# Kernel tuning notes

Hardware: AMD Instinct MI355X
Metric: run time of the kernel (lower is better)

The kernel has to match this reference:

```python
import jax, jax.numpy as jnp
import numpy as np

N_FREQ = 48  # tcnn Frequency encoding n_frequencies


def _freq_encode(x):
    # x: [N,3] in [0,1]; tcnn Frequency: sin/cos of x * 2^f * pi, f=0..F-1
    freqs = (2.0 ** jnp.arange(N_FREQ, dtype=jnp.float32)) * jnp.pi  # [F]
    ang = x[:, :, None] * freqs  # [N,3,F]
    enc = jnp.stack([jnp.sin(ang), jnp.cos(ang)], axis=-1)  # [N,3,F,2]
    return enc.reshape(x.shape[0], -1)  # [N, 3*F*2]


def _bilinear_sample(plane, coords):
    # plane: [R,R,F] (H,W,feat); coords: [N,2] in [-1,1], coords[:,0]->width(x), coords[:,1]->height(y)
    # matches torch grid_sample(align_corners=True, bilinear) for in-range coords
    R = plane.shape[0]
    gx = (coords[:, 0] + 1.0) * 0.5 * (R - 1)
    gy = (coords[:, 1] + 1.0) * 0.5 * (R - 1)
    x0f = jnp.clip(jnp.floor(gx), 0.0, R - 1)
    y0f = jnp.clip(jnp.floor(gy), 0.0, R - 1)
    x0 = x0f.astype(jnp.int32)
    y0 = y0f.astype(jnp.int32)
    x1 = jnp.minimum(x0 + 1, R - 1)
    y1 = jnp.minimum(y0 + 1, R - 1)
    wx = (gx - x0f)[:, None]
    wy = (gy - y0f)[:, None]
    v00 = plane[y0, x0]
    v01 = plane[y0, x1]
    v10 = plane[y1, x0]
    v11 = plane[y1, x1]
    return (v00 * (1 - wx) * (1 - wy) + v01 * wx * (1 - wy)
            + v10 * (1 - wx) * wy + v11 * wx * wy)  # [N,F]


def setup_inputs() -> dict:
    key = jax.random.key(0)
    ks = jax.random.split(key, 8)
    N = 524288
    res, fdim = 32, 16
    enc_dim = 3 * N_FREQ * 2  # 288
    d_in = enc_dim + fdim     # 304
    h = 64
    positions = jax.random.uniform(ks[0], (N, 3), dtype=jnp.float32)
    aabb = jnp.array([0.0, 0.0, 0.0, 1.0, 1.0, 1.0], dtype=jnp.float32)
    triplane = jax.random.normal(ks[1], (3, res, res, fdim), dtype=jnp.float32) * 0.001
    W0 = jax.random.normal(ks[2], (d_in, h), dtype=jnp.float32) / np.sqrt(d_in)
    W1 = jax.random.normal(ks[3], (h, h), dtype=jnp.float32) / np.sqrt(h)
    W2 = jax.random.normal(ks[4], (h, h), dtype=jnp.float32) / np.sqrt(h)
    W3 = jax.random.normal(ks[5], (h, 4), dtype=jnp.float32) / np.sqrt(h)
    return {"positions": positions, "aabb": aabb, "triplane": triplane,
            "W0": W0, "W1": W1, "W2": W2, "W3": W3}


def reference(positions, aabb, triplane, W0, W1, W2, W3):
    aabb_min, aabb_max = aabb[:3], aabb[3:]
    xn = (positions - aabb_min) / (aabb_max - aabb_min)          # normalized [0,1]
    sc = 2.0 * xn - 1.0                                          # scaled_coords in [-1,1]
    selector = jnp.all((xn > 0.0) & (xn < 1.0), axis=-1)
    # plane coordinate pairs as in the torch code
    coords = jnp.stack([
        jnp.stack([sc[:, 0], sc[:, 1]], axis=1),  # xy
        jnp.stack([sc[:, 0], sc[:, 2]], axis=1),  # xz
        jnp.stack([sc[:, 1], sc[:, 2]], axis=1),  # zy
    ], axis=0)  # [3,N,2]
    feats = jax.vmap(_bilinear_sample)(triplane, coords).sum(0)  # [N,fdim]
    h = jnp.concatenate([_freq_encode(xn), feats], axis=1)       # [N,304]
    h = jnp.sin(h @ W0)
    h = jnp.sin(h @ W1)
    h = jnp.sin(h @ W2)
    out = h @ W3                                                 # [N,4]
    rgb = jax.nn.sigmoid(out[:, :3])
    density = jnp.exp(out[:, 3:4] - 1.0) * selector[:, None]     # trunc_exp(x-1)
    return rgb, density
```

## Files before the change

kernel.cpp:

```cpp
#include <hip/hip_runtime.h>
#include <stdint.h>

typedef _Float16 half8  __attribute__((ext_vector_type(8)));
typedef _Float16 half2v __attribute__((ext_vector_type(2)));
typedef float f32x4 __attribute__((ext_vector_type(4)));

#define TPW 8
#define WPB 8
#define NT  512

__device__ __forceinline__ half2v pkrtz(float a, float b) {
    return __builtin_bit_cast(half2v, __builtin_amdgcn_cvt_pkrtz(a, b));
}

static __device__ __forceinline__ void wave_fence() {
    __builtin_amdgcn_wave_barrier();
    asm volatile("" ::: "memory");
}

__device__ __forceinline__ float bf2f(uint16_t u) {
    return __uint_as_float(((uint32_t)u) << 16);
}
__device__ __forceinline__ uint16_t f2bf(float f) {
    uint32_t u = __float_as_uint(f);
    u = (u + 0x7FFFu + ((u >> 16) & 1u)) >> 16;
    return (uint16_t)u;
}

template<bool BF>
__device__ __forceinline__ float lde(const void* p, uint32_t i) {
    if constexpr (BF) return bf2f(((const uint16_t*)p)[i]);
    else              return ((const float*)p)[i];
}
template<bool BF>
__device__ __forceinline__ void st1(void* p, uint32_t i, float v) {
    if constexpr (BF) ((uint16_t*)p)[i] = f2bf(v);
    else              ((float*)p)[i] = v;
}
template<bool BF>
__device__ __forceinline__ void ld8(const void* p, uint32_t i, float* o) {
    if constexpr (BF) {
        const uint4 c = *(const uint4*)((const uint16_t*)p + i);
        const uint32_t* pu = (const uint32_t*)&c;
#pragma unroll
        for (int j = 0; j < 4; ++j) {
            o[2 * j]     = __uint_as_float(pu[j] << 16);
            o[2 * j + 1] = __uint_as_float(pu[j] & 0xFFFF0000u);
        }
    } else {
        const float4 a = *(const float4*)((const float*)p + i);
        const float4 b = *(const float4*)((const float*)p + i + 4);
        o[0] = a.x; o[1] = a.y; o[2] = a.z; o[3] = a.w;
        o[4] = b.x; o[5] = b.y; o[6] = b.z; o[7] = b.w;
    }
}

__device__ __forceinline__ int hswz(int p, int g) {
    return p * 72 + ((g + 2 * (p >> 2)) & 7) * 8;
}

template<bool BF>
__device__ __forceinline__ void run_all(
    const void* __restrict__ posg, const void* __restrict__ aabbg,
    const void* __restrict__ tpg,
    const void* __restrict__ w0g, const void* __restrict__ w1g,
    const void* __restrict__ w2g, const void* __restrict__ w3g,
    void* __restrict__ outp, int npts,
    _Float16* w0t, _Float16* w1t, _Float16* w2t, _Float16* w3t, _Float16* hbuf)
{
    const int tid = threadIdx.x;
    const float I2PI = 0.15915494309189535f;

    for (int e = tid; e < 64 * 24; e += NT) { int n = e / 24, k = 304 + e % 24; w0t[n * 328 + k] = (_Float16)0.0f; }
    for (int e = tid; e < 4 * 72; e += NT) w3t[e] = (_Float16)0.0f;
    for (int e = tid; e < 304 * 64; e += NT) { int k = e >> 6, n = e & 63; w0t[n * 328 + k] = (_Float16)(lde<BF>(w0g, e) * I2PI); }
    for (int e = tid; e < 64 * 64;  e += NT) { int k = e >> 6, n = e & 63; w1t[n * 72 + k] = (_Float16)(lde<BF>(w1g, e) * I2PI);
                                               w2t[n * 72 + k] = (_Float16)(lde<BF>(w2g, e) * I2PI); }
    __syncthreads();
    for (int e = tid; e < 64 * 4;   e += NT) { int k = e >> 2, n = e & 3;  w3t[n * 72 + k] = (_Float16)lde<BF>(w3g, e); }
    __syncthreads();

    const int w = tid >> 6, lane = tid & 63;
    const int m = lane & 15, q = lane >> 4;
    _Float16* hb = hbuf + w * (16 * 72);

    const float mn0 = lde<BF>(aabbg, 0), mn1 = lde<BF>(aabbg, 1), mn2 = lde<BF>(aabbg, 2);
    const float mx0 = lde<BF>(aabbg, 3), mx1 = lde<BF>(aabbg, 4), mx2 = lde<BF>(aabbg, 5);

    const double IH = 0x1.45f306dc9c883p-2;
    const double IL = -0x1.6b01ec5417056p-56;
    const float PIF  = 3.14159274101257324f;
    const f32x4 z4 = {0.f, 0.f, 0.f, 0.f};

    const int tile0 = (blockIdx.x * WPB + w) * TPW;

    float cp0, cp1, cp2;
    {
        const int pt = tile0 * 16 + m;
        cp0 = lde<BF>(posg, 3 * pt + 0);
        cp1 = lde<BF>(posg, 3 * pt + 1);
        cp2 = lde<BF>(posg, 3 * pt + 2);
    }

    for (int it = 0; it < TPW; ++it) {
        const int base = (tile0 + it) * 16;
        const float p0 = cp0, p1 = cp1, p2 = cp2;
        {
            const int nit = (it + 1 < TPW) ? it + 1 : it;
            const int pt2 = (tile0 + nit) * 16 + m;
            cp0 = lde<BF>(posg, 3 * pt2 + 0);
            cp1 = lde<BF>(posg, 3 * pt2 + 1);
            cp2 = lde<BF>(posg, 3 * pt2 + 2);
        }

        float xn[3];
        xn[0] = (p0 - mn0) / (mx0 - mn0);
        xn[1] = (p1 - mn1) / (mx1 - mn1);
        xn[2] = (p2 - mn2) / (mx2 - mn2);

        const bool sel = xn[0] > 0.f && xn[0] < 1.f && xn[1] > 0.f && xn[1] < 1.f
                      && xn[2] > 0.f && xn[2] < 1.f;
        const unsigned long long bm = __ballot(sel);

        double wh[3], wl[3];
#pragma unroll
        for (int d = 0; d < 3; ++d) {
            const float mf = xn[d] * PIF;
            const double md = (double)mf;
            const double hi = md * IH;
            const double r  = __builtin_fma(md, IH, -hi);
            wh[d] = hi;
            wl[d] = __builtin_fma(md, IL, r);
        }

        float fe[8];
#pragma unroll
        for (int j = 0; j < 8; ++j) fe[j] = 0.f;
        if (q < 2) {
            const int fo = q * 8;
            float g[3];
#pragma unroll
            for (int d = 0; d < 3; ++d) g[d] = xn[d] * 31.f;
            float v[8];
#pragma unroll
            for (int p = 0; p < 3; ++p) {
                const float gx = (p == 2) ? g[1] : g[0];
                const float gy = (p == 0) ? g[1] : g[2];
                const float x0f = fminf(fmaxf(floorf(gx), 0.f), 31.f);
                const float y0f = fminf(fmaxf(floorf(gy), 0.f), 31.f);
                const int x0 = (int)x0f, y0 = (int)y0f;
                int x1 = x0 + 1; if (x1 > 31) x1 = 31;
                int y1 = y0 + 1; if (y1 > 31) y1 = 31;
                const float wx = gx - x0f, wy = gy - y0f;
                const float w00 = (1.f - wx) * (1.f - wy);
                const float w01 = wx * (1.f - wy);
                const float w10 = (1.f - wx) * wy;
                const float w11 = wx * wy;
                const uint32_t pb = p * 16384 + fo;
                ld8<BF>(tpg, pb + y0 * 512 + x0 * 16, v);
#pragma unroll
                for (int j = 0; j < 8; ++j) fe[j] += v[j] * w00;
                ld8<BF>(tpg, pb + y0 * 512 + x1 * 16, v);
#pragma unroll
                for (int j = 0; j < 8; ++j) fe[j] += v[j] * w01;
                ld8<BF>(tpg, pb + y1 * 512 + x0 * 16, v);
#pragma unroll
                for (int j = 0; j < 8; ++j) fe[j] += v[j] * w10;
                ld8<BF>(tpg, pb + y1 * 512 + x1 * 16, v);
#pragma unroll
                for (int j = 0; j < 8; ++j) fe[j] += v[j] * w11;
            }
        }

        f32x4 acc[4] = {z4, z4, z4, z4};
#pragma unroll
        for (int d = 0; d < 3; ++d) {
#pragma unroll
            for (int cc = 0; cc < 3; ++cc) {
                const int e0 = 16 * cc + 4 * q - 1;
                const double zp = __builtin_bit_cast(double, (uint64_t)(1023 + e0) << 52);
                const double z  = wh[d] * zp;
                const double zl = wl[d] * zp;
                const double fr = z - __builtin_floor(z);
                const float t = (float)(fr + zl);
                float s = __builtin_amdgcn_sinf(t);
                float c = __builtin_amdgcn_cosf(t);
                union { half8 h8; half2v h2[4]; } au;
                au.h2[0] = pkrtz(s, c);
#pragma unroll
                for (int jj = 1; jj < 4; ++jj) {
                    const float t2 = s + s;
                    const float sn = t2 * c;
                    c = __builtin_fmaf(-t2, s, 1.0f);
                    s = sn;
                    au.h2[jj] = pkrtz(s, c);
                }
                const int ch = 3 * d + cc;
#pragma unroll
                for (int t4 = 0; t4 < 4; ++t4) {
                    const half8 b = *(const half8*)&w0t[(t4 * 16 + m) * 328 + ch * 32 + q * 8];
                    acc[t4] = __builtin_amdgcn_mfma_f32_16x16x32_f16(au.h8, b, acc[t4], 0, 0, 0);
                }
            }
        }
        {
            union { half8 h8; half2v h2[4]; } au;
            if (q < 2) {
#pragma unroll
                for (int i = 0; i < 4; ++i)
                    au.h2[i] = pkrtz(fe[2 * i], fe[2 * i + 1]);
            } else {
#pragma unroll
                for (int j = 0; j < 8; ++j) au.h8[j] = (_Float16)0.f;
            }
#pragma unroll
            for (int t4 = 0; t4 < 4; ++t4) {
                const half8 b = *(const half8*)&w0t[(t4 * 16 + m) * 328 + 288 + q * 8];
                acc[t4] = __builtin_amdgcn_mfma_f32_16x16x32_f16(au.h8, b, acc[t4], 0, 0, 0);
            }
        }

#pragma unroll
        for (int t4 = 0; t4 < 4; ++t4) {
            const int gw = 2 * t4 + (m >> 3);
#pragma unroll
            for (int rg = 0; rg < 4; ++rg)
                hb[hswz(4 * q + rg, gw) + (m & 7)] =
                    (_Float16)__builtin_amdgcn_sinf(acc[t4][rg]);
        }
        wave_fence();

        f32x4 acc2[4] = {z4, z4, z4, z4};
#pragma unroll
        for (int c = 0; c < 2; ++c) {
            const half8 a = *(const half8*)&hb[hswz(m, 4 * c + q)];
#pragma unroll
            for (int t4 = 0; t4 < 4; ++t4) {
                const half8 b = *(const half8*)&w1t[(t4 * 16 + m) * 72 + c * 32 + q * 8];
                acc2[t4] = __builtin_amdgcn_mfma_f32_16x16x32_f16(a, b, acc2[t4], 0, 0, 0);
            }
        }
        wave_fence();
#pragma unroll
        for (int t4 = 0; t4 < 4; ++t4) {
            const int gw = 2 * t4 + (m >> 3);
#pragma unroll
            for (int rg = 0; rg < 4; ++rg)
                hb[hswz(4 * q + rg, gw) + (m & 7)] =
                    (_Float16)__builtin_amdgcn_sinf(acc2[t4][rg]);
        }
        wave_fence();

        f32x4 accx[4] = {z4, z4, z4, z4};
#pragma unroll
        for (int c = 0; c < 2; ++c) {
            const half8 a = *(const half8*)&hb[hswz(m, 4 * c + q)];
#pragma unroll
            for (int t4 = 0; t4 < 4; ++t4) {
                const half8 b = *(const half8*)&w2t[(t4 * 16 + m) * 72 + c * 32 + q * 8];
                accx[t4] = __builtin_amdgcn_mfma_f32_16x16x32_f16(a, b, accx[t4], 0, 0, 0);
            }
        }
        wave_fence();
#pragma unroll
        for (int t4 = 0; t4 < 4; ++t4) {
            const int gw = 2 * t4 + (m >> 3);
#pragma unroll
            for (int rg = 0; rg < 4; ++rg)
                hb[hswz(4 * q + rg, gw) + (m & 7)] =
                    (_Float16)__builtin_amdgcn_sinf(accx[t4][rg]);
        }
        wave_fence();

        f32x4 acc3 = z4;
#pragma unroll
        for (int c = 0; c < 2; ++c) {
            const half8 a = *(const half8*)&hb[hswz(m, 4 * c + q)];
            const half8 b = *(const half8*)&w3t[(m & 3) * 72 + c * 32 + q * 8];
            acc3 = __builtin_amdgcn_mfma_f32_16x16x32_f16(a, b, acc3, 0, 0, 0);
        }
        wave_fence();

        if (m < 3) {
#pragma unroll
            for (int rg = 0; rg < 4; ++rg) {
                const float s = 1.f / (1.f + __expf(-acc3[rg]));
                st1<BF>(outp, (uint32_t)(base + 4 * q + rg) * 3u + m, s);
            }
        } else if (m == 3) {
            float dv[4];
#pragma unroll
            for (int rg = 0; rg < 4; ++rg) {
                float dens = __expf(acc3[rg] - 1.f);
                if (!((bm >> (4 * q + rg)) & 1ull)) dens = 0.f;
                dv[rg] = dens;
            }
            const uint32_t di = 3u * (uint32_t)npts + (uint32_t)(base + 4 * q);
            if constexpr (BF) {
                ushort4 pk;
                pk.x = f2bf(dv[0]); pk.y = f2bf(dv[1]);
                pk.z = f2bf(dv[2]); pk.w = f2bf(dv[3]);
                *(ushort4*)((uint16_t*)outp + di) = pk;
            } else {
                float4 pk = {dv[0], dv[1], dv[2], dv[3]};
                *(float4*)((float*)outp + di) = pk;
            }
        }
    }
}

__global__ __launch_bounds__(NT, 2)
void tri_mlp(const void* __restrict__ posg, const void* __restrict__ aabbg,
             const void* __restrict__ tpg,
             const void* __restrict__ w0g, const void* __restrict__ w1g,
             const void* __restrict__ w2g, const void* __restrict__ w3g,
             void* __restrict__ outp, int npts)
{
    __shared__ alignas(16) _Float16 w0t[64 * 328];
    __shared__ alignas(16) _Float16 w1t[64 * 72];
    __shared__ alignas(16) _Float16 w2t[64 * 72];
    __shared__ alignas(16) _Float16 w3t[4 * 72];
    __shared__ alignas(16) _Float16 hbuf[WPB * 16 * 72];

    const bool bf = (((const uint32_t*)aabbg)[2] != 0u);
    if (bf) run_all<true >(posg, aabbg, tpg, w0g, w1g, w2g, w3g, outp, npts, w0t, w1t, w2t, w3t, hbuf);
    else    run_all<false>(posg, aabbg, tpg, w0g, w1g, w2g, w3g, outp, npts, w0t, w1t, w2t, w3t, hbuf);
}

extern "C" void kernel_launch(void* const* d_in, const int* in_sizes, int n_in,
                              void* d_out, int out_size, void* d_ws, size_t ws_size,
                              hipStream_t stream) {
    const int npts = in_sizes[0] / 3;
    const int blocks = npts / (16 * WPB * TPW);
    tri_mlp<<<blocks, NT, 0, stream>>>(d_in[0], d_in[1], d_in[2], d_in[3],
                                       d_in[4], d_in[5], d_in[6], d_out, npts);
}
```

Before: 146.6 us.

## Process two 16-point tiles per wave iteration to share weight loads

```diff
diff --git a/kernel.cpp b/kernel.cpp
--- a/kernel.cpp
+++ b/kernel.cpp
@@ -6,6 +6,7 @@
 typedef float f32x4 __attribute__((ext_vector_type(4)));
 
 #define TPW 8
+#define NPAIR 4
 #define WPB 8
 #define NT  512
 
@@ -82,7 +83,8 @@
 
     const int w = tid >> 6, lane = tid & 63;
     const int m = lane & 15, q = lane >> 4;
-    _Float16* hb = hbuf + w * (16 * 72);
+    _Float16* hb0 = hbuf + w * (32 * 72);
+    _Float16* hb1 = hb0 + 16 * 72;
 
     const float mn0 = lde<BF>(aabbg, 0), mn1 = lde<BF>(aabbg, 1), mn2 = lde<BF>(aabbg, 2);
     const float mx0 = lde<BF>(aabbg, 3), mx1 = lde<BF>(aabbg, 4), mx2 = lde<BF>(aabbg, 5);
@@ -94,216 +96,279 @@
 
     const int tile0 = (blockIdx.x * WPB + w) * TPW;
 
-    float cp0, cp1, cp2;
-    {
-        const int pt = tile0 * 16 + m;
-        cp0 = lde<BF>(posg, 3 * pt + 0);
-        cp1 = lde<BF>(posg, 3 * pt + 1);
-        cp2 = lde<BF>(posg, 3 * pt + 2);
+    float cp[2][3];
+#pragma unroll
+    for (int t = 0; t < 2; ++t) {
+        const int pt = (tile0 + t) * 16 + m;
+        cp[t][0] = lde<BF>(posg, 3 * pt + 0);
+        cp[t][1] = lde<BF>(posg, 3 * pt + 1);
+        cp[t][2] = lde<BF>(posg, 3 * pt + 2);
     }
 
-    for (int it = 0; it < TPW; ++it) {
-        const int base = (tile0 + it) * 16;
-        const float p0 = cp0, p1 = cp1, p2 = cp2;
+    for (int ip = 0; ip < NPAIR; ++ip) {
+        const int base0 = (tile0 + 2 * ip) * 16;
+
+        float px[2][3];
+#pragma unroll
+        for (int t = 0; t < 2; ++t) {
+            px[t][0] = cp[t][0]; px[t][1] = cp[t][1]; px[t][2] = cp[t][2];
+        }
         {
-            const int nit = (it + 1 < TPW) ? it + 1 : it;
-            const int pt2 = (tile0 + nit) * 16 + m;
-            cp0 = lde<BF>(posg, 3 * pt2 + 0);
-            cp1 = lde<BF>(posg, 3 * pt2 + 1);
-            cp2 = lde<BF>(posg, 3 * pt2 + 2);
-        }
-
-        float xn[3];
-        xn[0] = (p0 - mn0) / (mx0 - mn0);
-        xn[1] = (p1 - mn1) / (mx1 - mn1);
-        xn[2] = (p2 - mn2) / (mx2 - mn2);
-
-        const bool sel = xn[0] > 0.f && xn[0] < 1.f && xn[1] > 0.f && xn[1] < 1.f
-                      && xn[2] > 0.f && xn[2] < 1.f;
-        const unsigned long long bm = __ballot(sel);
-
-        double wh[3], wl[3];
-#pragma unroll
-        for (int d = 0; d < 3; ++d) {
-            const float mf = xn[d] * PIF;
-            const double md = (double)mf;
-            const double hi = md * IH;
-            const double r  = __builtin_fma(md, IH, -hi);
-            wh[d] = hi;
-            wl[d] = __builtin_fma(md, IL, r);
-        }
-
-        float fe[8];
-#pragma unroll
-        for (int j = 0; j < 8; ++j) fe[j] = 0.f;
+            const int nip = (ip + 1 < NPAIR) ? ip + 1 : ip;
+#pragma unroll
+            for (int t = 0; t < 2; ++t) {
+                const int pt2 = (tile0 + 2 * nip + t) * 16 + m;
+                cp[t][0] = lde<BF>(posg, 3 * pt2 + 0);
+                cp[t][1] = lde<BF>(posg, 3 * pt2 + 1);
+                cp[t][2] = lde<BF>(posg, 3 * pt2 + 2);
+            }
+        }
+
+        float xn[2][3];
+        unsigned long long bm[2];
+        double wh[2][3], wl[2][3];
+#pragma unroll
+        for (int t = 0; t < 2; ++t) {
+            xn[t][0] = (px[t][0] - mn0) / (mx0 - mn0);
+            xn[t][1] = (px[t][1] - mn1) / (mx1 - mn1);
+            xn[t][2] = (px[t][2] - mn2) / (mx2 - mn2);
+            const bool sel = xn[t][0] > 0.f && xn[t][0] < 1.f && xn[t][1] > 0.f
+                          && xn[t][1] < 1.f && xn[t][2] > 0.f && xn[t][2] < 1.f;
+            bm[t] = __ballot(sel);
+#pragma unroll
+            for (int d = 0; d < 3; ++d) {
+                const float mf = xn[t][d] * PIF;
+                const double md = (double)mf;
+                const double hi = md * IH;
+                const double r  = __builtin_fma(md, IH, -hi);
+                wh[t][d] = hi;
+                wl[t][d] = __builtin_fma(md, IL, r);
+            }
+        }
+
+        float fe[2][8];
+#pragma unroll
+        for (int t = 0; t < 2; ++t)
+#pragma unroll
+            for (int j = 0; j < 8; ++j) fe[t][j] = 0.f;
         if (q < 2) {
             const int fo = q * 8;
-            float g[3];
-#pragma unroll
-            for (int d = 0; d < 3; ++d) g[d] = xn[d] * 31.f;
-            float v[8];
-#pragma unroll
-            for (int p = 0; p < 3; ++p) {
-                const float gx = (p == 2) ? g[1] : g[0];
-                const float gy = (p == 0) ? g[1] : g[2];
-                const float x0f = fminf(fmaxf(floorf(gx), 0.f), 31.f);
-                const float y0f = fminf(fmaxf(floorf(gy), 0.f), 31.f);
-                const int x0 = (int)x0f, y0 = (int)y0f;
-                int x1 = x0 + 1; if (x1 > 31) x1 = 31;
-                int y1 = y0 + 1; if (y1 > 31) y1 = 31;
-                const float wx = gx - x0f, wy = gy - y0f;
-                const float w00 = (1.f - wx) * (1.f - wy);
-                const float w01 = wx * (1.f - wy);
-                const float w10 = (1.f - wx) * wy;
-                const float w11 = wx * wy;
-                const uint32_t pb = p * 16384 + fo;
-                ld8<BF>(tpg, pb + y0 * 512 + x0 * 16, v);
-#pragma unroll
-                for (int j = 0; j < 8; ++j) fe[j] += v[j] * w00;
-                ld8<BF>(tpg, pb + y0 * 512 + x1 * 16, v);
-#pragma unroll
-                for (int j = 0; j < 8; ++j) fe[j] += v[j] * w01;
-                ld8<BF>(tpg, pb + y1 * 512 + x0 * 16, v);
-#pragma unroll
-                for (int j = 0; j < 8; ++j) fe[j] += v[j] * w10;
-                ld8<BF>(tpg, pb + y1 * 512 + x1 * 16, v);
-#pragma unroll
-                for (int j = 0; j < 8; ++j) fe[j] += v[j] * w11;
-            }
-        }
-
-        f32x4 acc[4] = {z4, z4, z4, z4};
+#pragma unroll
+            for (int t = 0; t < 2; ++t) {
+                float g[3];
+#pragma unroll
+                for (int d = 0; d < 3; ++d) g[d] = xn[t][d] * 31.f;
+                float v[8];
+#pragma unroll
+                for (int p = 0; p < 3; ++p) {
+                    const float gx = (p == 2) ? g[1] : g[0];
+                    const float gy = (p == 0) ? g[1] : g[2];
+                    const float x0f = fminf(fmaxf(floorf(gx), 0.f), 31.f);
+                    const float y0f = fminf(fmaxf(floorf(gy), 0.f), 31.f);
+                    const int x0 = (int)x0f, y0 = (int)y0f;
+                    int x1 = x0 + 1; if (x1 > 31) x1 = 31;
+                    int y1 = y0 + 1; if (y1 > 31) y1 = 31;
+                    const float wx = gx - x0f, wy = gy - y0f;
+                    const float w00 = (1.f - wx) * (1.f - wy);
+                    const float w01 = wx * (1.f - wy);
+                    const float w10 = (1.f - wx) * wy;
+                    const float w11 = wx * wy;
+                    const uint32_t pb = p * 16384 + fo;
+                    ld8<BF>(tpg, pb + y0 * 512 + x0 * 16, v);
+#pragma unroll
+                    for (int j = 0; j < 8; ++j) fe[t][j] += v[j] * w00;
+                    ld8<BF>(tpg, pb + y0 * 512 + x1 * 16, v);
+#pragma unroll
+                    for (int j = 0; j < 8; ++j) fe[t][j] += v[j] * w01;
+                    ld8<BF>(tpg, pb + y1 * 512 + x0 * 16, v);
+#pragma unroll
+                    for (int j = 0; j < 8; ++j) fe[t][j] += v[j] * w10;
+                    ld8<BF>(tpg, pb + y1 * 512 + x1 * 16, v);
+#pragma unroll
+                    for (int j = 0; j < 8; ++j) fe[t][j] += v[j] * w11;
+                }
+            }
+        }
+
+        f32x4 acc[2][4];
+#pragma unroll
+        for (int t = 0; t < 2; ++t)
+#pragma unroll
+            for (int t4 = 0; t4 < 4; ++t4) acc[t][t4] = z4;
+
 #pragma unroll
         for (int d = 0; d < 3; ++d) {
 #pragma unroll
             for (int cc = 0; cc < 3; ++cc) {
                 const int e0 = 16 * cc + 4 * q - 1;
                 const double zp = __builtin_bit_cast(double, (uint64_t)(1023 + e0) << 52);
-                const double z  = wh[d] * zp;
-                const double zl = wl[d] * zp;
-                const double fr = z - __builtin_floor(z);
-                const float t = (float)(fr + zl);
-                float s = __builtin_amdgcn_sinf(t);
-                float c = __builtin_amdgcn_cosf(t);
-                union { half8 h8; half2v h2[4]; } au;
-                au.h2[0] = pkrtz(s, c);
-#pragma unroll
-                for (int jj = 1; jj < 4; ++jj) {
-                    const float t2 = s + s;
-                    const float sn = t2 * c;
-                    c = __builtin_fmaf(-t2, s, 1.0f);
-                    s = sn;
-                    au.h2[jj] = pkrtz(s, c);
+                half8 au[2];
+#pragma unroll
+                for (int t = 0; t < 2; ++t) {
+                    const double z  = wh[t][d] * zp;
+                    const double zl = wl[t][d] * zp;
+                    const double fr = z - __builtin_floor(z);
+                    const float tt = (float)(fr + zl);
+                    float s = __builtin_amdgcn_sinf(tt);
+                    float c = __builtin_amdgcn_cosf(tt);
+                    union { half8 h8; half2v h2[4]; } u;
+                    u.h2[0] = pkrtz(s, c);
+#pragma unroll
+                    for (int jj = 1; jj < 4; ++jj) {
+                        const float t2 = s + s;
+                        const float sn = t2 * c;
+                        c = __builtin_fmaf(-t2, s, 1.0f);
+                        s = sn;
+                        u.h2[jj] = pkrtz(s, c);
+                    }
+                    au[t] = u.h8;
                 }
                 const int ch = 3 * d + cc;
 #pragma unroll
                 for (int t4 = 0; t4 < 4; ++t4) {
                     const half8 b = *(const half8*)&w0t[(t4 * 16 + m) * 328 + ch * 32 + q * 8];
-                    acc[t4] = __builtin_amdgcn_mfma_f32_16x16x32_f16(au.h8, b, acc[t4], 0, 0, 0);
+                    acc[0][t4] = __builtin_amdgcn_mfma_f32_16x16x32_f16(au[0], b, acc[0][t4], 0, 0, 0);
+                    acc[1][t4] = __builtin_amdgcn_mfma_f32_16x16x32_f16(au[1], b, acc[1][t4], 0, 0, 0);
                 }
             }
         }
         {
-            union { half8 h8; half2v h2[4]; } au;
-            if (q < 2) {
-#pragma unroll
-                for (int i = 0; i < 4; ++i)
-                    au.h2[i] = pkrtz(fe[2 * i], fe[2 * i + 1]);
-            } else {
-#pragma unroll
-                for (int j = 0; j < 8; ++j) au.h8[j] = (_Float16)0.f;
+            half8 au[2];
+#pragma unroll
+            for (int t = 0; t < 2; ++t) {
+                union { half8 h8; half2v h2[4]; } u;
+                if (q < 2) {
+#pragma unroll
+                    for (int i = 0; i < 4; ++i)
+                        u.h2[i] = pkrtz(fe[t][2 * i], fe[t][2 * i + 1]);
+                } else {
+#pragma unroll
+                    for (int j = 0; j < 8; ++j) u.h8[j] = (_Float16)0.f;
+                }
+                au[t] = u.h8;
             }
 #pragma unroll
             for (int t4 = 0; t4 < 4; ++t4) {
                 const half8 b = *(const half8*)&w0t[(t4 * 16 + m) * 328 + 288 + q * 8];
-                acc[t4] = __builtin_amdgcn_mfma_f32_16x16x32_f16(au.h8, b, acc[t4], 0, 0, 0);
-            }
-        }
-
-#pragma unroll
-        for (int t4 = 0; t4 < 4; ++t4) {
-            const int gw = 2 * t4 + (m >> 3);
-#pragma unroll
-            for (int rg = 0; rg < 4; ++rg)
-                hb[hswz(4 * q + rg, gw) + (m & 7)] =
-                    (_Float16)__builtin_amdgcn_sinf(acc[t4][rg]);
-        }
-        wave_fence();
-
-        f32x4 acc2[4] = {z4, z4, z4, z4};
+                acc[0][t4] = __builtin_amdgcn_mfma_f32_16x16x32_f16(au[0], b, acc[0][t4], 0, 0, 0);
+                acc[1][t4] = __builtin_amdgcn_mfma_f32_16x16x32_f16(au[1], b, acc[1][t4], 0, 0, 0);
+            }
+        }
+
+#pragma unroll
+        for (int t = 0; t < 2; ++t) {
+            _Float16* hb = t ? hb1 : hb0;
+#pragma unroll
+            for (int t4 = 0; t4 < 4; ++t4) {
+                const int gw = 2 * t4 + (m >> 3);
+#pragma unroll
+                for (int rg = 0; rg < 4; ++rg)
+                    hb[hswz(4 * q + rg, gw) + (m & 7)] =
+                        (_Float16)__builtin_amdgcn_sinf(acc[t][t4][rg]);
+            }
+        }
+        wave_fence();
+
+        f32x4 acc2[2][4];
+#pragma unroll
+        for (int t = 0; t < 2; ++t)
+#pragma unroll
+            for (int t4 = 0; t4 < 4; ++t4) acc2[t][t4] = z4;
 #pragma unroll
         for (int c = 0; c < 2; ++c) {
-            const half8 a = *(const half8*)&hb[hswz(m, 4 * c + q)];
+            const half8 aA = *(const half8*)&hb0[hswz(m, 4 * c + q)];
+            const half8 aB = *(const half8*)&hb1[hswz(m, 4 * c + q)];
 #pragma unroll
             for (int t4 = 0; t4 < 4; ++t4) {
                 const half8 b = *(const half8*)&w1t[(t4 * 16 + m) * 72 + c * 32 + q * 8];
-                acc2[t4] = __builtin_amdgcn_mfma_f32_16x16x32_f16(a, b, acc2[t4], 0, 0, 0);
-            }
-        }
-        wave_fence();
-#pragma unroll
-        for (int t4 = 0; t4 < 4; ++t4) {
-            const int gw = 2 * t4 + (m >> 3);
-#pragma unroll
-            for (int rg = 0; rg < 4; ++rg)
-                hb[hswz(4 * q + rg, gw) + (m & 7)] =
-                    (_Float16)__builtin_amdgcn_sinf(acc2[t4][rg]);
-        }
-        wave_fence();
-
-        f32x4 accx[4] = {z4, z4, z4, z4};
+                acc2[0][t4] = __builtin_amdgcn_mfma_f32_16x16x32_f16(aA, b, acc2[0][t4], 0, 0, 0);
+                acc2[1][t4] = __builtin_amdgcn_mfma_f32_16x16x32_f16(aB, b, acc2[1][t4], 0, 0, 0);
+            }
+        }
+        wave_fence();
+#pragma unroll
+        for (int t = 0; t < 2; ++t) {
+            _Float16* hb = t ? hb1 : hb0;
+#pragma unroll
+            for (int t4 = 0; t4 < 4; ++t4) {
+                const int gw = 2 * t4 + (m >> 3);
+#pragma unroll
+                for (int rg = 0; rg < 4; ++rg)
+                    hb[hswz(4 * q + rg, gw) + (m & 7)] =
+                        (_Float16)__builtin_amdgcn_sinf(acc2[t][t4][rg]);
+            }
+        }
+        wave_fence();
+
+        f32x4 accx[2][4];
+#pragma unroll
+        for (int t = 0; t < 2; ++t)
+#pragma unroll
+            for (int t4 = 0; t4 < 4; ++t4) accx[t][t4] = z4;
 #pragma unroll
         for (int c = 0; c < 2; ++c) {
-            const half8 a = *(const half8*)&hb[hswz(m, 4 * c + q)];
+            const half8 aA = *(const half8*)&hb0[hswz(m, 4 * c + q)];
+            const half8 aB = *(const half8*)&hb1[hswz(m, 4 * c + q)];
 #pragma unroll
             for (int t4 = 0; t4 < 4; ++t4) {
                 const half8 b = *(const half8*)&w2t[(t4 * 16 + m) * 72 + c * 32 + q * 8];
-                accx[t4] = __builtin_amdgcn_mfma_f32_16x16x32_f16(a, b, accx[t4], 0, 0, 0);
-            }
-        }
-        wave_fence();
-#pragma unroll
-        for (int t4 = 0; t4 < 4; ++t4) {
-            const int gw = 2 * t4 + (m >> 3);
-#pragma unroll
-            for (int rg = 0; rg < 4; ++rg)
-                hb[hswz(4 * q + rg, gw) + (m & 7)] =
-                    (_Float16)__builtin_amdgcn_sinf(accx[t4][rg]);
-        }
-        wave_fence();
-
-        f32x4 acc3 = z4;
+                accx[0][t4] = __builtin_amdgcn_mfma_f32_16x16x32_f16(aA, b, accx[0][t4], 0, 0, 0);
+                accx[1][t4] = __builtin_amdgcn_mfma_f32_16x16x32_f16(aB, b, accx[1][t4], 0, 0, 0);
+            }
+        }
+        wave_fence();
+#pragma unroll
+        for (int t = 0; t < 2; ++t) {
+            _Float16* hb = t ? hb1 : hb0;
+#pragma unroll
+            for (int t4 = 0; t4 < 4; ++t4) {
+                const int gw = 2 * t4 + (m >> 3);
+#pragma unroll
+                for (int rg = 0; rg < 4; ++rg)
+                    hb[hswz(4 * q + rg, gw) + (m & 7)] =
+                        (_Float16)__builtin_amdgcn_sinf(accx[t][t4][rg]);
+            }
+        }
+        wave_fence();
+
+        f32x4 acc3[2] = {z4, z4};
 #pragma unroll
         for (int c = 0; c < 2; ++c) {
-            const half8 a = *(const half8*)&hb[hswz(m, 4 * c + q)];
+            const half8 aA = *(const half8*)&hb0[hswz(m, 4 * c + q)];
+            const half8 aB = *(const half8*)&hb1[hswz(m, 4 * c + q)];
             const half8 b = *(const half8*)&w3t[(m & 3) * 72 + c * 32 + q * 8];
-            acc3 = __builtin_amdgcn_mfma_f32_16x16x32_f16(a, b, acc3, 0, 0, 0);
-        }
-        wave_fence();
-
-        if (m < 3) {
-#pragma unroll
-            for (int rg = 0; rg < 4; ++rg) {
-                const float s = 1.f / (1.f + __expf(-acc3[rg]));
-                st1<BF>(outp, (uint32_t)(base + 4 * q + rg) * 3u + m, s);
-            }
-        } else if (m == 3) {
-            float dv[4];
-#pragma unroll
-            for (int rg = 0; rg < 4; ++rg) {
-                float dens = __expf(acc3[rg] - 1.f);
-                if (!((bm >> (4 * q + rg)) & 1ull)) dens = 0.f;
-                dv[rg] = dens;
-            }
-            const uint32_t di = 3u * (uint32_t)npts + (uint32_t)(base + 4 * q);
-            if constexpr (BF) {
-                ushort4 pk;
-                pk.x = f2bf(dv[0]); pk.y = f2bf(dv[1]);
-                pk.z = f2bf(dv[2]); pk.w = f2bf(dv[3]);
-                *(ushort4*)((uint16_t*)outp + di) = pk;
-            } else {
-                float4 pk = {dv[0], dv[1], dv[2], dv[3]};
-                *(float4*)((float*)outp + di) = pk;
+            acc3[0] = __builtin_amdgcn_mfma_f32_16x16x32_f16(aA, b, acc3[0], 0, 0, 0);
+            acc3[1] = __builtin_amdgcn_mfma_f32_16x16x32_f16(aB, b, acc3[1], 0, 0, 0);
+        }
+        wave_fence();
+
+#pragma unroll
+        for (int t = 0; t < 2; ++t) {
+            const int base = base0 + t * 16;
+            if (m < 3) {
+#pragma unroll
+                for (int rg = 0; rg < 4; ++rg) {
+                    const float s = 1.f / (1.f + __expf(-acc3[t][rg]));
+                    st1<BF>(outp, (uint32_t)(base + 4 * q + rg) * 3u + m, s);
+                }
+            } else if (m == 3) {
+                float dv[4];
+#pragma unroll
+                for (int rg = 0; rg < 4; ++rg) {
+                    float dens = __expf(acc3[t][rg] - 1.f);
+                    if (!((bm[t] >> (4 * q + rg)) & 1ull)) dens = 0.f;
+                    dv[rg] = dens;
+                }
+                const uint32_t di = 3u * (uint32_t)npts + (uint32_t)(base + 4 * q);
+                if constexpr (BF) {
+                    ushort4 pk;
+                    pk.x = f2bf(dv[0]); pk.y = f2bf(dv[1]);
+                    pk.z = f2bf(dv[2]); pk.w = f2bf(dv[3]);
+                    *(ushort4*)((uint16_t*)outp + di) = pk;
+                } else {
+                    float4 pk = {dv[0], dv[1], dv[2], dv[3]};
+                    *(float4*)((float*)outp + di) = pk;
+                }
             }
         }
     }
@@ -320,7 +385,7 @@
     __shared__ alignas(16) _Float16 w1t[64 * 72];
     __shared__ alignas(16) _Float16 w2t[64 * 72];
     __shared__ alignas(16) _Float16 w3t[4 * 72];
-    __shared__ alignas(16) _Float16 hbuf[WPB * 16 * 72];
+    __shared__ alignas(16) _Float16 hbuf[WPB * 32 * 72];
 
     const bool bf = (((const uint32_t*)aabbg)[2] != 0u);
     if (bf) run_all<true >(posg, aabbg, tpg, w0g, w1g, w2g, w3g, outp, npts, w0t, w1t, w2t, w3t, hbuf);
```

After: 146.6 us. About the same (+0.0%).

## Software-pipeline layer-0 encoding of next tile with MLP tail of current tile

Applied to the files above, without the earlier changes.

```diff
diff --git a/kernel.cpp b/kernel.cpp
--- a/kernel.cpp
+++ b/kernel.cpp
@@ -11,11 +11,6 @@
 
 __device__ __forceinline__ half2v pkrtz(float a, float b) {
     return __builtin_bit_cast(half2v, __builtin_amdgcn_cvt_pkrtz(a, b));
-}
-
-static __device__ __forceinline__ void wave_fence() {
-    __builtin_amdgcn_wave_barrier();
-    asm volatile("" ::: "memory");
 }
 
 __device__ __forceinline__ float bf2f(uint16_t u) {
@@ -82,7 +77,8 @@
 
     const int w = tid >> 6, lane = tid & 63;
     const int m = lane & 15, q = lane >> 4;
-    _Float16* hb = hbuf + w * (16 * 72);
+    _Float16* hbA = hbuf + w * (2 * 16 * 72);
+    _Float16* hbB = hbA + 16 * 72;
 
     const float mn0 = lde<BF>(aabbg, 0), mn1 = lde<BF>(aabbg, 1), mn2 = lde<BF>(aabbg, 2);
     const float mx0 = lde<BF>(aabbg, 3), mx1 = lde<BF>(aabbg, 4), mx2 = lde<BF>(aabbg, 5);
@@ -102,12 +98,11 @@
         cp2 = lde<BF>(posg, 3 * pt + 2);
     }
 
-    for (int it = 0; it < TPW; ++it) {
-        const int base = (tile0 + it) * 16;
+    auto encL0 = [&](int j, f32x4* acc, unsigned long long& bmo) {
         const float p0 = cp0, p1 = cp1, p2 = cp2;
         {
-            const int nit = (it + 1 < TPW) ? it + 1 : it;
-            const int pt2 = (tile0 + nit) * 16 + m;
+            const int nj = (j + 1 < TPW) ? j + 1 : j;
+            const int pt2 = (tile0 + nj) * 16 + m;
             cp0 = lde<BF>(posg, 3 * pt2 + 0);
             cp1 = lde<BF>(posg, 3 * pt2 + 1);
             cp2 = lde<BF>(posg, 3 * pt2 + 2);
@@ -120,7 +115,7 @@
 
         const bool sel = xn[0] > 0.f && xn[0] < 1.f && xn[1] > 0.f && xn[1] < 1.f
                       && xn[2] > 0.f && xn[2] < 1.f;
-        const unsigned long long bm = __ballot(sel);
+        bmo = __ballot(sel);
 
         double wh[3], wl[3];
 #pragma unroll
@@ -135,7 +130,7 @@
 
         float fe[8];
 #pragma unroll
-        for (int j = 0; j < 8; ++j) fe[j] = 0.f;
+        for (int jj = 0; jj < 8; ++jj) fe[jj] = 0.f;
         if (q < 2) {
             const int fo = q * 8;
             float g[3];
@@ -159,20 +154,20 @@
                 const uint32_t pb = p * 16384 + fo;
                 ld8<BF>(tpg, pb + y0 * 512 + x0 * 16, v);
 #pragma unroll
-                for (int j = 0; j < 8; ++j) fe[j] += v[j] * w00;
+                for (int jj = 0; jj < 8; ++jj) fe[jj] += v[jj] * w00;
                 ld8<BF>(tpg, pb + y0 * 512 + x1 * 16, v);
 #pragma unroll
-                for (int j = 0; j < 8; ++j) fe[j] += v[j] * w01;
+                for (int jj = 0; jj < 8; ++jj) fe[jj] += v[jj] * w01;
                 ld8<BF>(tpg, pb + y1 * 512 + x0 * 16, v);
 #pragma unroll
-                for (int j = 0; j < 8; ++j) fe[j] += v[j] * w10;
+                for (int jj = 0; jj < 8; ++jj) fe[jj] += v[jj] * w10;
                 ld8<BF>(tpg, pb + y1 * 512 + x1 * 16, v);
 #pragma unroll
-                for (int j = 0; j < 8; ++j) fe[j] += v[j] * w11;
-            }
-        }
-
-        f32x4 acc[4] = {z4, z4, z4, z4};
+                for (int jj = 0; jj < 8; ++jj) fe[jj] += v[jj] * w11;
+            }
+        }
+
+        acc[0] = z4; acc[1] = z4; acc[2] = z4; acc[3] = z4;
 #pragma unroll
         for (int d = 0; d < 3; ++d) {
 #pragma unroll
@@ -207,11 +202,11 @@
             union { half8 h8; half2v h2[4]; } au;
             if (q < 2) {
 #pragma unroll
-                for (int i = 0; i < 4; ++i)
-                    au.h2[i] = pkrtz(fe[2 * i], fe[2 * i + 1]);
+                for (int i2 = 0; i2 < 4; ++i2)
+                    au.h2[i2] = pkrtz(fe[2 * i2], fe[2 * i2 + 1]);
             } else {
 #pragma unroll
-                for (int j = 0; j < 8; ++j) au.h8[j] = (_Float16)0.f;
+                for (int jj = 0; jj < 8; ++jj) au.h8[jj] = (_Float16)0.f;
             }
 #pragma unroll
             for (int t4 = 0; t4 < 4; ++t4) {
@@ -219,6 +214,16 @@
                 acc[t4] = __builtin_amdgcn_mfma_f32_16x16x32_f16(au.h8, b, acc[t4], 0, 0, 0);
             }
         }
+    };
+
+    f32x4 accA[4];
+    unsigned long long bmA;
+    encL0(0, accA, bmA);
+
+#pragma unroll 2
+    for (int i = 0; i < TPW; ++i) {
+        _Float16* hb = (i & 1) ? hbB : hbA;
+        const int base = (tile0 + i) * 16;
 
 #pragma unroll
         for (int t4 = 0; t4 < 4; ++t4) {
@@ -226,9 +231,12 @@
 #pragma unroll
             for (int rg = 0; rg < 4; ++rg)
                 hb[hswz(4 * q + rg, gw) + (m & 7)] =
-                    (_Float16)__builtin_amdgcn_sinf(acc[t4][rg]);
-        }
-        wave_fence();
+                    (_Float16)__builtin_amdgcn_sinf(accA[t4][rg]);
+        }
+
+        f32x4 accN[4] = {z4, z4, z4, z4};
+        unsigned long long bmN = 0;
+        if (i + 1 < TPW) encL0(i + 1, accN, bmN);
 
         f32x4 acc2[4] = {z4, z4, z4, z4};
 #pragma unroll
@@ -240,7 +248,6 @@
                 acc2[t4] = __builtin_amdgcn_mfma_f32_16x16x32_f16(a, b, acc2[t4], 0, 0, 0);
             }
         }
-        wave_fence();
 #pragma unroll
         for (int t4 = 0; t4 < 4; ++t4) {
             const int gw = 2 * t4 + (m >> 3);
@@ -249,7 +256,6 @@
                 hb[hswz(4 * q + rg, gw) + (m & 7)] =
                     (_Float16)__builtin_amdgcn_sinf(acc2[t4][rg]);
         }
-        wave_fence();
 
         f32x4 accx[4] = {z4, z4, z4, z4};
 #pragma unroll
@@ -261,7 +267,6 @@
                 accx[t4] = __builtin_amdgcn_mfma_f32_16x16x32_f16(a, b, accx[t4], 0, 0, 0);
             }
         }
-        wave_fence();
 #pragma unroll
         for (int t4 = 0; t4 < 4; ++t4) {
             const int gw = 2 * t4 + (m >> 3);
@@ -270,7 +275,6 @@
                 hb[hswz(4 * q + rg, gw) + (m & 7)] =
                     (_Float16)__builtin_amdgcn_sinf(accx[t4][rg]);
         }
-        wave_fence();
 
         f32x4 acc3 = z4;
 #pragma unroll
@@ -279,7 +283,6 @@
             const half8 b = *(const half8*)&w3t[(m & 3) * 72 + c * 32 + q * 8];
             acc3 = __builtin_amdgcn_mfma_f32_16x16x32_f16(a, b, acc3, 0, 0, 0);
         }
-        wave_fence();
 
         if (m < 3) {
 #pragma unroll
@@ -292,7 +295,7 @@
 #pragma unroll
             for (int rg = 0; rg < 4; ++rg) {
                 float dens = __expf(acc3[rg] - 1.f);
-                if (!((bm >> (4 * q + rg)) & 1ull)) dens = 0.f;
+                if (!((bmA >> (4 * q + rg)) & 1ull)) dens = 0.f;
                 dv[rg] = dens;
             }
             const uint32_t di = 3u * (uint32_t)npts + (uint32_t)(base + 4 * q);
@@ -306,6 +309,10 @@
                 *(float4*)((float*)outp + di) = pk;
             }
         }
+
+#pragma unroll
+        for (int t4 = 0; t4 < 4; ++t4) accA[t4] = accN[t4];
+        bmA = bmN;
     }
 }
 
@@ -320,7 +327,7 @@
     __shared__ alignas(16) _Float16 w1t[64 * 72];
     __shared__ alignas(16) _Float16 w2t[64 * 72];
     __shared__ alignas(16) _Float16 w3t[4 * 72];
-    __shared__ alignas(16) _Float16 hbuf[WPB * 16 * 72];
+    __shared__ alignas(16) _Float16 hbuf[WPB * 2 * 16 * 72];
 
     const bool bf = (((const uint32_t*)aabbg)[2] != 0u);
     if (bf) run_all<true >(posg, aabbg, tpg, w0g, w1g, w2g, w3g, outp, npts, w0t, w1t, w2t, w3t, hbuf);
```

After: 147.8 us. About the same (+0.9%).
